# Kernel tuning notes

Hardware: AMD Instinct MI355X
Metric: run time of the kernel (lower is better)

Reference implementation:

```python
import jax, jax.numpy as jnp
import numpy as np

B = 512
IN_F, HID, OUT_F = 342, 512, 311


def setup_inputs() -> dict:
    key = jax.random.key(0)
    ks = jax.random.split(key, 8)
    return {
        "p": jax.random.uniform(ks[0], (B,), dtype=jnp.float32),
        "x": jax.random.normal(ks[1], (B, IN_F), dtype=jnp.float32),
        "W0": jax.random.normal(ks[2], (4, IN_F, HID), dtype=jnp.float32) * 0.05,
        "b0": jax.random.normal(ks[3], (4, HID), dtype=jnp.float32) * 0.05,
        "W1": jax.random.normal(ks[4], (4, HID, HID), dtype=jnp.float32) * 0.05,
        "b1": jax.random.normal(ks[5], (4, HID), dtype=jnp.float32) * 0.05,
        "W2": jax.random.normal(ks[6], (4, HID, OUT_F), dtype=jnp.float32) * 0.05,
        "b2": jax.random.normal(ks[7], (4, OUT_F), dtype=jnp.float32) * 0.05,
    }


def _cubic(y0, y1, y2, y3, mu, mu2, mu3):
    # Catmull-Rom cubic interpolation (same coefficients as the torch module)
    return ((-0.5 * y0 + 1.5 * y1 - 1.5 * y2 + 0.5 * y3) * mu3
            + (y0 - 2.5 * y1 + 2.0 * y2 - 0.5 * y3) * mu2
            + (-0.5 * y0 + 0.5 * y2) * mu
            + y1)


def reference(p, x, W0, b0, W1, b1, W2, b2):
    p4 = p * 4.0
    pa = jnp.mod(p4, 1.0)                      # (B,) fractional phase
    i1 = p4.astype(jnp.int32) % 4              # (B,) control point indices
    i0 = (i1 - 1) % 4
    i2 = (i1 + 1) % 4
    i3 = (i1 + 2) % 4

    wa = pa[:, None, None]                     # (B,1,1) for weights
    wa2, wa3 = wa * wa, wa * wa * wa
    ba = pa[:, None]                           # (B,1) for biases
    ba2, ba3 = ba * ba, ba * ba * ba

    def interp_w(W):  # W: (4, din, dout) -> (B, din, dout)
        return _cubic(W[i0], W[i1], W[i2], W[i3], wa, wa2, wa3)

    def interp_b(b):  # b: (4, d) -> (B, d)
        return _cubic(b[i0], b[i1], b[i2], b[i3], ba, ba2, ba3)

    h = jax.nn.elu(jnp.einsum('bi,bio->bo', x, interp_w(W0)) + interp_b(b0))
    h = jax.nn.elu(jnp.einsum('bi,bio->bo', h, interp_w(W1)) + interp_b(b1))
    y = jnp.einsum('bi,bio->bo', h, interp_w(W2)) + interp_b(b2)
    return y
```

## Files before the change

kernel.cpp:

```cpp
#include <hip/hip_runtime.h>
#include <math.h>

typedef __bf16 bf16x8 __attribute__((ext_vector_type(8)));
typedef float f32x4 __attribute__((ext_vector_type(4)));

#define B_SZ 512
#define IN_F 342
#define HID  512
#define OUT_F 311

template <int JOB>
__device__ void wt_transpose(const float* __restrict__ W, __bf16* __restrict__ T,
                             int t) {
  constexpr int KP   = (JOB == 0) ? 384 : 512;
  constexpr int KWF  = (JOB == 0) ? IN_F : HID;
  constexpr int NC   = (JOB == 2) ? OUT_F : HID;
  constexpr int NSUB = (JOB == 2) ? 320 : 512;
  constexpr int KT   = KP / 64;
  const int r0 = (t / KT) * 64, k0 = (t % KT) * 64;
  __shared__ __bf16 tile[64][66];
  const int tid = threadIdx.x;
  const int rl = tid & 63;
  const int c = r0 / NSUB;
  const int nbase = r0 - c * NSUB;
#pragma unroll
  for (int jj = 0; jj < 16; ++jj) {
    int kl = (tid >> 6) + jj * 4;
    int k = k0 + kl;
    int n = nbase + rl;
    float v = 0.0f;
    if ((JOB != 0 || k < KWF) && (JOB != 2 || n < NC))
      v = W[((size_t)c * KWF + k) * NC + n];
    tile[rl][kl] = (__bf16)v;
  }
  __syncthreads();
  int row = tid >> 2, o0 = (tid & 3) * 16;
  bf16x8 v0 = *(const bf16x8*)&tile[row][o0];
  bf16x8 v1 = *(const bf16x8*)&tile[row][o0 + 8];
  int g = (nbase + row) * 4 + c;
  __bf16* dst = T + (size_t)g * KP + k0 + o0;
  *(bf16x8*)dst = v0;
  *(bf16x8*)(dst + 8) = v1;
}

template <int LAYER>
__device__ void gemm_body(int nx, int my, const __bf16* __restrict__ A,
                          const __bf16* __restrict__ BT,
                          const float* __restrict__ bias,
                          const float* __restrict__ coef,
                          void* __restrict__ outv) {
  constexpr int KA = (LAYER == 0) ? 384 : 512;
  constexpr int T = KA / 128;
  constexpr int LDA = 136;
  constexpr int ASZ = 32 * LDA;
  constexpr int BSZ = 64 * LDA;
  __shared__ __bf16 Als[2 * ASZ];
  __shared__ __bf16 Bls[2 * BSZ];

  const int tid = threadIdx.x;
  const int l = tid & 63;
  const int wave = tid >> 6;
  const int wm = wave >> 1, wn = wave & 1;
  const int lr = l & 15, lk = l >> 4;
  const int m0 = my * 32;
  const int n0 = nx * 64;

  const int ar = tid >> 3, ao = tid & 7;
  const int br = tid >> 2, bo = tid & 3;

  const __bf16* Ap = A + (size_t)(m0 + ar) * KA + ao * 8;
  const __bf16* Bp = BT + (size_t)(n0 + br) * KA + bo * 16;

  bf16x8 a0_, a1_, b0_, b1_, b2_, b3_;
  f32x4 acc[2] = {};

  auto loadreg = [&](int t) {
    a0_ = *(const bf16x8*)&Ap[t * 128];
    a1_ = *(const bf16x8*)&Ap[t * 128 + 64];
    b0_ = *(const bf16x8*)&Bp[t * 128];
    b1_ = *(const bf16x8*)&Bp[t * 128 + 8];
    b2_ = *(const bf16x8*)&Bp[t * 128 + 64];
    b3_ = *(const bf16x8*)&Bp[t * 128 + 72];
  };
  auto storeLDS = [&](int ph) {
    __bf16* Ac = Als + ph * ASZ;
    __bf16* Bc = Bls + ph * BSZ;
    *(bf16x8*)&Ac[ar * LDA + ao * 8] = a0_;
    *(bf16x8*)&Ac[ar * LDA + ao * 8 + 64] = a1_;
    *(bf16x8*)&Bc[br * LDA + bo * 16] = b0_;
    *(bf16x8*)&Bc[br * LDA + bo * 16 + 8] = b1_;
    *(bf16x8*)&Bc[br * LDA + bo * 16 + 64] = b2_;
    *(bf16x8*)&Bc[br * LDA + bo * 16 + 72] = b3_;
  };
  auto compute = [&](int ph) {
    const __bf16* Ac = Als + ph * ASZ;
    const __bf16* Bc = Bls + ph * BSZ;
#pragma unroll
    for (int kk = 0; kk < 128; kk += 32) {
      bf16x8 af = *(const bf16x8*)&Ac[(wm * 16 + lr) * LDA + kk + lk * 8];
      bf16x8 bg[2];
#pragma unroll
      for (int j = 0; j < 2; ++j)
        bg[j] = *(const bf16x8*)&Bc[(wn * 32 + j * 16 + lr) * LDA + kk + lk * 8];
#pragma unroll
      for (int j = 0; j < 2; ++j)
        acc[j] = __builtin_amdgcn_mfma_f32_16x16x32_bf16(af, bg[j], acc[j], 0, 0, 0);
    }
  };

  loadreg(0);
  storeLDS(0);
  __syncthreads();
  for (int t = 0; t < T; ++t) {
    if (t + 1 < T) loadreg(t + 1);
    compute(t & 1);
    if (t + 1 < T) {
      storeLDS((t + 1) & 1);
      __syncthreads();
    }
  }

  const int cl = l & 3;
#pragma unroll
  for (int j = 0; j < 2; ++j) {
    int gnp = n0 + wn * 32 + j * 16 + lr;
    int hn = gnp >> 2;
    float bv;
    if (LAYER == 2) bv = (hn < OUT_F) ? bias[cl * OUT_F + hn] : 0.0f;
    else            bv = bias[cl * HID + hn];
#pragma unroll
    for (int r = 0; r < 4; ++r) {
      int gm = m0 + wm * 16 + lk * 4 + r;
      float cf = coef[gm * 4 + cl];
      float v = cf * (acc[j][r] + bv);
      v += __shfl_xor(v, 1);
      v += __shfl_xor(v, 2);
      if (LAYER == 2) {
        if (cl == 0 && hn < OUT_F)
          ((float*)outv)[(size_t)gm * OUT_F + hn] = v;
      } else {
        if (cl == 0) {
          float e = (v > 0.0f) ? v : expm1f(v);
          ((__bf16*)outv)[(size_t)gm * HID + hn] = (__bf16)e;
        }
      }
    }
  }
}

__global__ __launch_bounds__(256) void setup_kernel(
    const float* __restrict__ p, const float* __restrict__ x,
    const float* __restrict__ W0, const float* __restrict__ W1,
    const float* __restrict__ W2, float* __restrict__ coef,
    __bf16* __restrict__ A0, __bf16* __restrict__ T0,
    __bf16* __restrict__ T1, __bf16* __restrict__ T2) {
  int bid = blockIdx.x, tid = threadIdx.x;
  if (bid < 192)      { wt_transpose<0>(W0, T0, bid); return; }
  if (bid < 448)      { wt_transpose<1>(W1, T1, bid - 192); return; }
  if (bid < 608)      { wt_transpose<2>(W2, T2, bid - 448); return; }
  if (bid < 624) {
    int base = (bid - 608) * 32;
    for (int e = tid; e < 32 * 384; e += 256) {
      int m = base + e / 384, i = e - (e / 384) * 384;
      A0[(size_t)m * 384 + i] =
          (i < IN_F) ? (__bf16)x[(size_t)m * IN_F + i] : (__bf16)0.0f;
    }
    return;
  }
  for (int b = tid; b < B_SZ; b += 256) {
    float p4 = p[b] * 4.0f;
    float mu = p4 - floorf(p4);
    int i1 = ((int)p4) & 3;
    float mu2 = mu * mu, mu3 = mu2 * mu;
    float c0 = -0.5f * mu3 + mu2 - 0.5f * mu;
    float c1 =  1.5f * mu3 - 2.5f * mu2 + 1.0f;
    float c2 = -1.5f * mu3 + 2.0f * mu2 + 0.5f * mu;
    float c3 =  0.5f * mu3 - 0.5f * mu2;
    float arr[4];
    arr[(i1 + 3) & 3] = c0;
    arr[i1]           = c1;
    arr[(i1 + 1) & 3] = c2;
    arr[(i1 + 2) & 3] = c3;
    coef[b * 4 + 0] = arr[0];
    coef[b * 4 + 1] = arr[1];
    coef[b * 4 + 2] = arr[2];
    coef[b * 4 + 3] = arr[3];
  }
}

__global__ __launch_bounds__(256) void g0_kernel(
    const __bf16* __restrict__ A0, const __bf16* __restrict__ T0,
    const float* __restrict__ b0, const float* __restrict__ coef,
    __bf16* __restrict__ E1) {
  gemm_body<0>(blockIdx.x, blockIdx.y, A0, T0, b0, coef, E1);
}

__global__ __launch_bounds__(256) void g1_kernel(
    const __bf16* __restrict__ E1, const __bf16* __restrict__ T1,
    const float* __restrict__ b1, const float* __restrict__ coef,
    __bf16* __restrict__ E2) {
  gemm_body<1>(blockIdx.x, blockIdx.y, E1, T1, b1, coef, E2);
}

__global__ __launch_bounds__(256) void g2_kernel(
    const __bf16* __restrict__ E2, const __bf16* __restrict__ T2,
    const float* __restrict__ b2, const float* __restrict__ coef,
    float* __restrict__ out) {
  gemm_body<2>(blockIdx.x, blockIdx.y, E2, T2, b2, coef, out);
}

extern "C" void kernel_launch(void* const* d_in, const int* in_sizes, int n_in,
                              void* d_out, int out_size, void* d_ws, size_t ws_size,
                              hipStream_t stream) {
  const float* p  = (const float*)d_in[0];
  const float* x  = (const float*)d_in[1];
  const float* W0 = (const float*)d_in[2];
  const float* b0 = (const float*)d_in[3];
  const float* W1 = (const float*)d_in[4];
  const float* b1 = (const float*)d_in[5];
  const float* W2 = (const float*)d_in[6];
  const float* b2 = (const float*)d_in[7];
  float* out = (float*)d_out;

  char* w = (char*)d_ws;
  float*  coef = (float*)w;   w += 8192;
  __bf16* A0   = (__bf16*)w;  w += (size_t)B_SZ * 384 * 2;
  __bf16* T0   = (__bf16*)w;  w += (size_t)2048 * 384 * 2;
  __bf16* T1   = (__bf16*)w;  w += (size_t)2048 * 512 * 2;
  __bf16* T2   = (__bf16*)w;  w += (size_t)1280 * 512 * 2;
  __bf16* E1   = (__bf16*)w;  w += (size_t)B_SZ * HID * 2;
  __bf16* E2   = (__bf16*)w;  w += (size_t)B_SZ * HID * 2;

  setup_kernel<<<625, 256, 0, stream>>>(p, x, W0, W1, W2, coef, A0, T0, T1, T2);
  g0_kernel<<<dim3(32, 16), 256, 0, stream>>>(A0, T0, b0, coef, E1);
  g1_kernel<<<dim3(32, 16), 256, 0, stream>>>(E1, T1, b1, coef, E2);
  g2_kernel<<<dim3(20, 16), 256, 0, stream>>>(E2, T2, b2, coef, out);
}
```

Measured before the change: 42.45 us.

## Shrink GEMM tiles to 32x32 and load full K into LDS at once

Each GEMM block now computes a 32x32 output tile instead of 32x64, doubling the grid to put more blocks on the GPU. It also drops the double-buffered K pipeline: the whole K extent of A and B is loaded into shared memory in one step with a single barrier, and the MFMAs then run back to back. This aims to raise occupancy and parallelism for these small GEMMs and to remove per-step barriers. In exchange, each block uses more LDS, each wave issues only one MFMA chain, and global loads no longer overlap compute.

```diff
diff --git a/kernel.cpp b/kernel.cpp
--- a/kernel.cpp
+++ b/kernel.cpp
@@ -50,12 +50,10 @@
                           const float* __restrict__ coef,
                           void* __restrict__ outv) {
   constexpr int KA = (LAYER == 0) ? 384 : 512;
-  constexpr int T = KA / 128;
-  constexpr int LDA = 136;
-  constexpr int ASZ = 32 * LDA;
-  constexpr int BSZ = 64 * LDA;
-  __shared__ __bf16 Als[2 * ASZ];
-  __shared__ __bf16 Bls[2 * BSZ];
+  constexpr int NL = KA / 64;
+  constexpr int LDK = KA + 8;
+  __shared__ __bf16 Als[32 * LDK];
+  __shared__ __bf16 Bls[32 * LDK];
 
   const int tid = threadIdx.x;
   const int l = tid & 63;
@@ -63,86 +61,54 @@
   const int wm = wave >> 1, wn = wave & 1;
   const int lr = l & 15, lk = l >> 4;
   const int m0 = my * 32;
-  const int n0 = nx * 64;
-
-  const int ar = tid >> 3, ao = tid & 7;
-  const int br = tid >> 2, bo = tid & 3;
-
-  const __bf16* Ap = A + (size_t)(m0 + ar) * KA + ao * 8;
-  const __bf16* Bp = BT + (size_t)(n0 + br) * KA + bo * 16;
-
-  bf16x8 a0_, a1_, b0_, b1_, b2_, b3_;
-  f32x4 acc[2] = {};
-
-  auto loadreg = [&](int t) {
-    a0_ = *(const bf16x8*)&Ap[t * 128];
-    a1_ = *(const bf16x8*)&Ap[t * 128 + 64];
-    b0_ = *(const bf16x8*)&Bp[t * 128];
-    b1_ = *(const bf16x8*)&Bp[t * 128 + 8];
-    b2_ = *(const bf16x8*)&Bp[t * 128 + 64];
-    b3_ = *(const bf16x8*)&Bp[t * 128 + 72];
-  };
-  auto storeLDS = [&](int ph) {
-    __bf16* Ac = Als + ph * ASZ;
-    __bf16* Bc = Bls + ph * BSZ;
-    *(bf16x8*)&Ac[ar * LDA + ao * 8] = a0_;
-    *(bf16x8*)&Ac[ar * LDA + ao * 8 + 64] = a1_;
-    *(bf16x8*)&Bc[br * LDA + bo * 16] = b0_;
-    *(bf16x8*)&Bc[br * LDA + bo * 16 + 8] = b1_;
-    *(bf16x8*)&Bc[br * LDA + bo * 16 + 64] = b2_;
-    *(bf16x8*)&Bc[br * LDA + bo * 16 + 72] = b3_;
-  };
-  auto compute = [&](int ph) {
-    const __bf16* Ac = Als + ph * ASZ;
-    const __bf16* Bc = Bls + ph * BSZ;
-#pragma unroll
-    for (int kk = 0; kk < 128; kk += 32) {
-      bf16x8 af = *(const bf16x8*)&Ac[(wm * 16 + lr) * LDA + kk + lk * 8];
-      bf16x8 bg[2];
-#pragma unroll
-      for (int j = 0; j < 2; ++j)
-        bg[j] = *(const bf16x8*)&Bc[(wn * 32 + j * 16 + lr) * LDA + kk + lk * 8];
-#pragma unroll
-      for (int j = 0; j < 2; ++j)
-        acc[j] = __builtin_amdgcn_mfma_f32_16x16x32_bf16(af, bg[j], acc[j], 0, 0, 0);
-    }
-  };
-
-  loadreg(0);
-  storeLDS(0);
+  const int n0 = nx * 32;
+
+  const int r_ = tid >> 3;
+  const int o_ = tid & 7;
+  const __bf16* Ap = A + (size_t)(m0 + r_) * KA + o_ * 8;
+  const __bf16* Bp = BT + (size_t)(n0 + r_) * KA + o_ * 8;
+
+  bf16x8 av[NL], bv[NL];
+#pragma unroll
+  for (int j = 0; j < NL; ++j) av[j] = *(const bf16x8*)&Ap[j * 64];
+#pragma unroll
+  for (int j = 0; j < NL; ++j) bv[j] = *(const bf16x8*)&Bp[j * 64];
+#pragma unroll
+  for (int j = 0; j < NL; ++j)
+    *(bf16x8*)&Als[r_ * LDK + o_ * 8 + j * 64] = av[j];
+#pragma unroll
+  for (int j = 0; j < NL; ++j)
+    *(bf16x8*)&Bls[r_ * LDK + o_ * 8 + j * 64] = bv[j];
   __syncthreads();
-  for (int t = 0; t < T; ++t) {
-    if (t + 1 < T) loadreg(t + 1);
-    compute(t & 1);
-    if (t + 1 < T) {
-      storeLDS((t + 1) & 1);
-      __syncthreads();
-    }
+
+  f32x4 acc = {};
+#pragma unroll
+  for (int kk = 0; kk < KA; kk += 32) {
+    bf16x8 af = *(const bf16x8*)&Als[(wm * 16 + lr) * LDK + kk + lk * 8];
+    bf16x8 bg = *(const bf16x8*)&Bls[(wn * 16 + lr) * LDK + kk + lk * 8];
+    acc = __builtin_amdgcn_mfma_f32_16x16x32_bf16(af, bg, acc, 0, 0, 0);
   }
 
   const int cl = l & 3;
-#pragma unroll
-  for (int j = 0; j < 2; ++j) {
-    int gnp = n0 + wn * 32 + j * 16 + lr;
-    int hn = gnp >> 2;
-    float bv;
-    if (LAYER == 2) bv = (hn < OUT_F) ? bias[cl * OUT_F + hn] : 0.0f;
-    else            bv = bias[cl * HID + hn];
-#pragma unroll
-    for (int r = 0; r < 4; ++r) {
-      int gm = m0 + wm * 16 + lk * 4 + r;
-      float cf = coef[gm * 4 + cl];
-      float v = cf * (acc[j][r] + bv);
-      v += __shfl_xor(v, 1);
-      v += __shfl_xor(v, 2);
-      if (LAYER == 2) {
-        if (cl == 0 && hn < OUT_F)
-          ((float*)outv)[(size_t)gm * OUT_F + hn] = v;
-      } else {
-        if (cl == 0) {
-          float e = (v > 0.0f) ? v : expm1f(v);
-          ((__bf16*)outv)[(size_t)gm * HID + hn] = (__bf16)e;
-        }
+  int gnp = n0 + wn * 16 + lr;
+  int hn = gnp >> 2;
+  float bv_;
+  if (LAYER == 2) bv_ = (hn < OUT_F) ? bias[cl * OUT_F + hn] : 0.0f;
+  else            bv_ = bias[cl * HID + hn];
+#pragma unroll
+  for (int r = 0; r < 4; ++r) {
+    int gm = m0 + wm * 16 + lk * 4 + r;
+    float cf = coef[gm * 4 + cl];
+    float v = cf * (acc[r] + bv_);
+    v += __shfl_xor(v, 1);
+    v += __shfl_xor(v, 2);
+    if (LAYER == 2) {
+      if (cl == 0 && hn < OUT_F)
+        ((float*)outv)[(size_t)gm * OUT_F + hn] = v;
+    } else {
+      if (cl == 0) {
+        float e = (v > 0.0f) ? v : expm1f(v);
+        ((__bf16*)outv)[(size_t)gm * HID + hn] = (__bf16)e;
       }
     }
   }
@@ -232,7 +198,7 @@
   __bf16* E2   = (__bf16*)w;  w += (size_t)B_SZ * HID * 2;
 
   setup_kernel<<<625, 256, 0, stream>>>(p, x, W0, W1, W2, coef, A0, T0, T1, T2);
-  g0_kernel<<<dim3(32, 16), 256, 0, stream>>>(A0, T0, b0, coef, E1);
-  g1_kernel<<<dim3(32, 16), 256, 0, stream>>>(E1, T1, b1, coef, E2);
-  g2_kernel<<<dim3(20, 16), 256, 0, stream>>>(E2, T2, b2, coef, out);
-}
+  g0_kernel<<<dim3(64, 16), 256, 0, stream>>>(A0, T0, b0, coef, E1);
+  g1_kernel<<<dim3(64, 16), 256, 0, stream>>>(E1, T1, b1, coef, E2);
+  g2_kernel<<<dim3(40, 16), 256, 0, stream>>>(E2, T2, b2, coef, out);
+}
```

Result: slower. 43.89 us (+3.4%).
